# Optimization experiments

Hardware: AMD Instinct MI355X
Metric: run time of the kernel (lower is better)

Reference implementation:

```python
import jax, jax.numpy as jnp
import numpy as np

B, L, T = 256, 256, 50  # batch, max_len, num_tags


def setup_inputs() -> dict:
    key = jax.random.key(0)
    k1, k2, k3 = jax.random.split(key, 3)
    feats = jax.random.normal(k1, (B, L, T), dtype=jnp.float32)
    trans_m = jax.random.normal(k2, (T, T), dtype=jnp.float32)
    tags = jax.random.randint(k3, (B, L), 0, T)
    mask = jnp.ones((B, L), dtype=jnp.int32)
    return {"feats": feats, "trans_m": trans_m, "tags": tags, "mask": mask}


def _normalizer(logits, trans_m, m):
    # logits: (L, B, T), m: (L, B) float mask
    alpha0 = logits[0]  # (B, T)

    def step(alpha, inp):
        emit, mt = inp  # (B, T), (B,)
        # (B, T_from, T_to) broadcast add, logsumexp over T_from
        tmp = alpha[:, :, None] + trans_m[None, :, :] + emit[:, None, :]
        new = jax.nn.logsumexp(tmp, axis=1)
        alpha = jnp.where(mt[:, None] > 0, new, alpha)
        return alpha, None

    alpha, _ = jax.lax.scan(step, alpha0, (logits[1:], m[1:]))
    return jax.nn.logsumexp(alpha, axis=1)  # (B,)


def _gold_score(logits, trans_m, tags_t, m):
    # logits: (L, B, T); tags_t: (L, B); m: (L, B)
    trans_sc = trans_m[tags_t[:-1], tags_t[1:]] * m[1:]  # (L-1, B)
    emit_sc = jnp.take_along_axis(logits, tags_t[:, :, None], axis=2)[..., 0] * m  # (L, B)
    return jnp.sum(trans_sc + emit_sc[:-1], axis=0) + emit_sc[-1]  # (B,)


def reference(feats, trans_m, tags, mask):
    # feats: (B, L, T) -> (L, B, T); include_start_end_trans=False
    logits = jnp.transpose(feats, (1, 0, 2))
    tags_t = tags.T
    m = mask.T.astype(feats.dtype)
    all_path = _normalizer(logits, trans_m, m)
    gold = _gold_score(logits, trans_m, tags_t, m)
    return all_path - gold  # (B,) loss per example
```

## Files before the change

### kernel.cpp

```cpp
#include <hip/hip_runtime.h>
#include <math.h>


#define TAGS 50
#define LEN 256
#define NB 256
#define VST 32
#define NCH 6
#define CST 32
#define INV_LN2 1.4426950408889634f
#define LN2 0.6931471805599453f

typedef __attribute__((ext_vector_type(8))) short bf16x8;
typedef __attribute__((ext_vector_type(4))) float f32x4;

#if __has_builtin(__builtin_amdgcn_exp2f)
#define EXP2F(x) __builtin_amdgcn_exp2f(x)
#else
#define EXP2F(x) exp2f(x)
#endif
#if __has_builtin(__builtin_amdgcn_logf)
#define LOG2F(x) __builtin_amdgcn_logf(x)
#else
#define LOG2F(x) log2f(x)
#endif
#if __has_builtin(__builtin_amdgcn_rcpf)
#define RCPF(x) __builtin_amdgcn_rcpf(x)
#else
#define RCPF(x) (1.0f / (x))
#endif

__device__ __forceinline__ float readlane_f(float v, int srclane) {
  return __builtin_bit_cast(float,
      __builtin_amdgcn_readlane(__builtin_bit_cast(int, v), srclane));
}

__device__ __forceinline__ int bfpack(float lo, float hi) {
  unsigned lb = __builtin_bit_cast(unsigned, lo) + 0x8000u;
  unsigned hb = __builtin_bit_cast(unsigned, hi) + 0x8000u;
#if __has_builtin(__builtin_amdgcn_perm)
  return (int)__builtin_amdgcn_perm(hb, lb, 0x07060302u);
#else
  return (int)((hb & 0xFFFF0000u) | (lb >> 16));
#endif
}

union U8 { int i[4]; bf16x8 v; };

#define WS_U(b)    ((b) * 64)
#define WS_W(b)    ((NB + (b)) * 64)
#define WS_SF(b)   (2 * NB * 64 + (b))
#define WS_SB(b)   (2 * NB * 64 + NB + (b))
#define WS_SC(b,c) (2 * NB * 64 + 2 * NB + (b) * NCH + (c))
#define WS_T(b,c)  (2 * NB * 64 + 2 * NB + NB * NCH + (((b) * NCH + (c)) * 64) * 64)

__global__ __launch_bounds__(64, 1) void crf_scan_kernel(
    const float* __restrict__ feats,
    const float* __restrict__ trans,
    const int*   __restrict__ mask,
    float*       __restrict__ ws)
{
  const int bid  = blockIdx.x;
  const int lane = threadIdx.x;
  const int q    = lane >> 4;
  const int n    = lane & 15;
  const f32x4 zero4 = {0.0f, 0.0f, 0.0f, 0.0f};

  if (bid < 2 * NB) {
    const bool is_fwd = bid < NB;
    const int b = is_fwd ? bid : bid - NB;

    __shared__ __align__(16) float fl[VST * TAGS];
    __shared__ int ml[VST];

    const int base_l = is_fwd ? 0 : (LEN - VST);
    const float* fb = feats + ((size_t)b * LEN + base_l) * TAGS;
    const int*   mb = mask + b * LEN + base_l;

    {
      const float4* fv = (const float4*)fb;
      for (int i = lane; i < (VST * TAGS) / 4; i += 64) {
        float4 v4 = fv[i];
        v4.x *= INV_LN2; v4.y *= INV_LN2; v4.z *= INV_LN2; v4.w *= INV_LN2;
        *(float4*)&fl[i * 4] = v4;
      }
      for (int i = lane; i < VST; i += 64) ml[i] = mb[i];
    }

    int tcl[4], vld[4];
#pragma unroll
    for (int t = 0; t < 4; ++t) {
      const int tg = n + 16 * t;
      vld[t] = tg < TAGS;
      tcl[t] = vld[t] ? tg : (TAGS - 1);
    }

    U8 Bfr[4][2];
#pragma unroll
    for (int t = 0; t < 4; ++t)
#pragma unroll
      for (int c = 0; c < 2; ++c)
#pragma unroll
        for (int r = 0; r < 4; ++r) {
          const int col = 16 * t + n;
          const int tag0 = 16 * c + 4 * q + r;
          const int tag1 = tag0 + 32;
          float e0 = 0.0f, e1 = 0.0f;
          if (col < TAGS) {
            if (tag0 < TAGS)
              e0 = EXP2F((is_fwd ? trans[tag0 * TAGS + col]
                                 : trans[col * TAGS + tag0]) * INV_LN2);
            if (tag1 < TAGS)
              e1 = EXP2F((is_fwd ? trans[tag1 * TAGS + col]
                                 : trans[col * TAGS + tag1]) * INV_LN2);
          }
          Bfr[t][c].i[r] = bfpack(e0, e1);
        }

    int addr[4];
#pragma unroll
    for (int r = 0; r < 4; ++r) addr[r] = (4 * q + r) * 4;

    __syncthreads();

    float v[4], S;
    if (is_fwd) {
      const float c0 = fl[0];
#pragma unroll
      for (int t = 0; t < 4; ++t) v[t] = vld[t] ? EXP2F(fl[tcl[t]] - c0) : 0.0f;
      S = c0;
      float eh[4];
#pragma unroll
      for (int t = 0; t < 4; ++t) eh[t] = EXP2F(fl[TAGS + tcl[t]]);
      int m_nxt = ml[1];

      for (int l = 1; l < VST; ++l) {
        const int m_cur = m_nxt;
        const int ln = (l + 1 < VST) ? (l + 1) : (VST - 1);
        const int P0 = bfpack(v[0], v[2]);
        const int P1 = bfpack(v[1], v[3]);
        const float cc = readlane_f(v[0], 0);
        const float rr = RCPF(cc);
        U8 A0, A1;
#pragma unroll
        for (int r = 0; r < 4; ++r) {
          A0.i[r] = __builtin_amdgcn_ds_bpermute(addr[r], P0);
          A1.i[r] = __builtin_amdgcn_ds_bpermute(addr[r], P1);
        }
        f32x4 d0 = __builtin_amdgcn_mfma_f32_16x16x32_bf16(A0.v, Bfr[0][0].v, zero4, 0, 0, 0);
        f32x4 d1 = __builtin_amdgcn_mfma_f32_16x16x32_bf16(A0.v, Bfr[1][0].v, zero4, 0, 0, 0);
        f32x4 d2 = __builtin_amdgcn_mfma_f32_16x16x32_bf16(A0.v, Bfr[2][0].v, zero4, 0, 0, 0);
        f32x4 d3 = __builtin_amdgcn_mfma_f32_16x16x32_bf16(A0.v, Bfr[3][0].v, zero4, 0, 0, 0);
        f32x4 g0 = __builtin_amdgcn_mfma_f32_16x16x32_bf16(A1.v, Bfr[0][1].v, zero4, 0, 0, 0);
        f32x4 g1 = __builtin_amdgcn_mfma_f32_16x16x32_bf16(A1.v, Bfr[1][1].v, zero4, 0, 0, 0);
        f32x4 g2 = __builtin_amdgcn_mfma_f32_16x16x32_bf16(A1.v, Bfr[2][1].v, zero4, 0, 0, 0);
        f32x4 g3 = __builtin_amdgcn_mfma_f32_16x16x32_bf16(A1.v, Bfr[3][1].v, zero4, 0, 0, 0);
        float ehn[4];
#pragma unroll
        for (int t = 0; t < 4; ++t) ehn[t] = fl[ln * TAGS + tcl[t]];
        const int m_n2 = ml[ln];
        v[0] = ((m_cur > 0) ? (d0[0] + g0[0]) * eh[0] : v[0]) * rr;
        v[1] = ((m_cur > 0) ? (d1[0] + g1[0]) * eh[1] : v[1]) * rr;
        v[2] = ((m_cur > 0) ? (d2[0] + g2[0]) * eh[2] : v[2]) * rr;
        v[3] = ((m_cur > 0) ? (d3[0] + g3[0]) * eh[3] : v[3]) * rr;
        S += LOG2F(cc);
#pragma unroll
        for (int t = 0; t < 4; ++t) eh[t] = EXP2F(ehn[t]);
        m_nxt = m_n2;
      }
      if (lane < 16) {
#pragma unroll
        for (int t = 0; t < 4; ++t) ws[WS_U(b) + n + 16 * t] = v[t];
      }
      if (lane == 0) ws[WS_SF(b)] = S;
    } else {
#pragma unroll
      for (int t = 0; t < 4; ++t) v[t] = vld[t] ? 1.0f : 0.0f;
      S = 0.0f;
      float eh[4];
#pragma unroll
      for (int t = 0; t < 4; ++t) eh[t] = EXP2F(fl[(VST - 1) * TAGS + tcl[t]]);
      int m_nxt = ml[VST - 1];

      for (int l = VST - 1; l >= 0; --l) {
        const int m_cur = m_nxt;
        const int ln = (l > 0) ? (l - 1) : 0;
        const float x0 = v[0] * eh[0];
        const float x1 = v[1] * eh[1];
        const float x2 = v[2] * eh[2];
        const float x3 = v[3] * eh[3];
        const int P0 = bfpack(x0, x2);
        const int P1 = bfpack(x1, x3);
        const float cc = readlane_f(v[0], 0);
        const float rr = RCPF(cc);
        U8 A0, A1;
#pragma unroll
        for (int r = 0; r < 4; ++r) {
          A0.i[r] = __builtin_amdgcn_ds_bpermute(addr[r], P0);
          A1.i[r] = __builtin_amdgcn_ds_bpermute(addr[r], P1);
        }
        f32x4 d0 = __builtin_amdgcn_mfma_f32_16x16x32_bf16(A0.v, Bfr[0][0].v, zero4, 0, 0, 0);
        f32x4 d1 = __builtin_amdgcn_mfma_f32_16x16x32_bf16(A0.v, Bfr[1][0].v, zero4, 0, 0, 0);
        f32x4 d2 = __builtin_amdgcn_mfma_f32_16x16x32_bf16(A0.v, Bfr[2][0].v, zero4, 0, 0, 0);
        f32x4 d3 = __builtin_amdgcn_mfma_f32_16x16x32_bf16(A0.v, Bfr[3][0].v, zero4, 0, 0, 0);
        f32x4 g0 = __builtin_amdgcn_mfma_f32_16x16x32_bf16(A1.v, Bfr[0][1].v, zero4, 0, 0, 0);
        f32x4 g1 = __builtin_amdgcn_mfma_f32_16x16x32_bf16(A1.v, Bfr[1][1].v, zero4, 0, 0, 0);
        f32x4 g2 = __builtin_amdgcn_mfma_f32_16x16x32_bf16(A1.v, Bfr[2][1].v, zero4, 0, 0, 0);
        f32x4 g3 = __builtin_amdgcn_mfma_f32_16x16x32_bf16(A1.v, Bfr[3][1].v, zero4, 0, 0, 0);
        float ehn[4];
#pragma unroll
        for (int t = 0; t < 4; ++t) ehn[t] = fl[ln * TAGS + tcl[t]];
        const int m_n2 = ml[ln];
        v[0] = ((m_cur > 0) ? (d0[0] + g0[0]) : v[0]) * rr;
        v[1] = ((m_cur > 0) ? (d1[0] + g1[0]) : v[1]) * rr;
        v[2] = ((m_cur > 0) ? (d2[0] + g2[0]) : v[2]) * rr;
        v[3] = ((m_cur > 0) ? (d3[0] + g3[0]) : v[3]) * rr;
        S += LOG2F(cc);
#pragma unroll
        for (int t = 0; t < 4; ++t) eh[t] = EXP2F(ehn[t]);
        m_nxt = m_n2;
      }
      if (lane < 16) {
#pragma unroll
        for (int t = 0; t < 4; ++t) ws[WS_W(b) + n + 16 * t] = v[t];
      }
      if (lane == 0) ws[WS_SB(b)] = S;
    }
    return;
  }

  {
    const int i2 = bid - 2 * NB;
    const int b = i2 / NCH;
    const int cidx = i2 - b * NCH;
    const int l0 = CST * (cidx + 1);

    __shared__ __align__(16) float em[CST * 52 + 16];
    __shared__ int ml[CST];

    for (int i = lane; i < CST * 52 + 16; i += 64) em[i] = 0.0f;
    __syncthreads();

    const float* fbc = feats + ((size_t)b * LEN + l0) * TAGS;
    {
      const float4* fv = (const float4*)fbc;
      for (int i = lane; i < (CST * TAGS) / 4; i += 64) {
        const float4 v4 = fv[i];
        const int g = i * 4;
#pragma unroll
        for (int e = 0; e < 4; ++e) {
          const int gg = g + e;
          const int row = gg / TAGS;
          const int col = gg - row * TAGS;
          const float val = (e == 0) ? v4.x : (e == 1) ? v4.y : (e == 2) ? v4.z : v4.w;
          em[row * 52 + col] = val * INV_LN2;
        }
      }
      for (int i = lane; i < CST; i += 64) ml[i] = mask[b * LEN + l0 + i];
    }

    U8 Afr[4][2];
#pragma unroll
    for (int tm = 0; tm < 4; ++tm)
#pragma unroll
      for (int c2 = 0; c2 < 2; ++c2)
#pragma unroll
        for (int rr = 0; rr < 4; ++rr) {
          const int m = 16 * tm + n;
          const int kr = 32 * c2 + 16 * (rr >> 1) + 4 * q + 2 * (rr & 1);
          const float e0 = (m < TAGS && kr < TAGS)
              ? EXP2F(trans[kr * TAGS + m] * INV_LN2) : 0.0f;
          const float e1 = (m < TAGS && kr + 1 < TAGS)
              ? EXP2F(trans[(kr + 1) * TAGS + m] * INV_LN2) : 0.0f;
          Afr[tm][c2].i[rr] = bfpack(e0, e1);
        }

    __syncthreads();

    f32x4 d[4][4];
#pragma unroll
    for (int tm = 0; tm < 4; ++tm)
#pragma unroll
      for (int tn = 0; tn < 4; ++tn)
#pragma unroll
        for (int e = 0; e < 4; ++e)
          d[tm][tn][e] = (tm == tn && n == 4 * q + e) ? 1.0f : 0.0f;

    float S = 0.0f;

    for (int l = 0; l < CST; ++l) {
      if (ml[l] > 0) {
        const float cc = readlane_f(d[0][0][0], 0);
        const float rv = RCPF(cc);

        U8 Bf[2][4];
#pragma unroll
        for (int c2 = 0; c2 < 2; ++c2)
#pragma unroll
          for (int tn = 0; tn < 4; ++tn) {
            Bf[c2][tn].i[0] = bfpack(d[2 * c2][tn][0], d[2 * c2][tn][1]);
            Bf[c2][tn].i[1] = bfpack(d[2 * c2][tn][2], d[2 * c2][tn][3]);
            Bf[c2][tn].i[2] = bfpack(d[2 * c2 + 1][tn][0], d[2 * c2 + 1][tn][1]);
            Bf[c2][tn].i[3] = bfpack(d[2 * c2 + 1][tn][2], d[2 * c2 + 1][tn][3]);
          }

        float sc[4][4];
#pragma unroll
        for (int tm = 0; tm < 4; ++tm) {
          const f32x4 er = *(const f32x4*)&em[l * 52 + 16 * tm + 4 * q];
#pragma unroll
          for (int e = 0; e < 4; ++e) sc[tm][e] = EXP2F(er[e]) * rv;
        }

#pragma unroll
        for (int tm = 0; tm < 4; ++tm)
#pragma unroll
          for (int tn = 0; tn < 4; ++tn) {
            f32x4 acc = __builtin_amdgcn_mfma_f32_16x16x32_bf16(
                Afr[tm][0].v, Bf[0][tn].v, zero4, 0, 0, 0);
            acc = __builtin_amdgcn_mfma_f32_16x16x32_bf16(
                Afr[tm][1].v, Bf[1][tn].v, acc, 0, 0, 0);
#pragma unroll
            for (int e = 0; e < 4; ++e) d[tm][tn][e] = acc[e] * sc[tm][e];
          }
        S += LOG2F(cc);
      }
    }

    float* tw = ws + WS_T(b, cidx);
#pragma unroll
    for (int tm = 0; tm < 4; ++tm)
#pragma unroll
      for (int tn = 0; tn < 4; ++tn)
#pragma unroll
        for (int e = 0; e < 4; ++e)
          tw[(16 * tn + n) * 64 + 16 * tm + 4 * q + e] = d[tm][tn][e];
    if (lane == 0) ws[WS_SC(b, cidx)] = S;
  }
}

__global__ __launch_bounds__(64) void crf_combine_kernel(
    const float* __restrict__ feats,
    const float* __restrict__ trans,
    const int*   __restrict__ tags,
    const int*   __restrict__ mask,
    const float* __restrict__ ws,
    float*       __restrict__ out)
{
  const int b = blockIdx.x;
  const int lane = threadIdx.x;

  float x = ws[WS_U(b) + lane];
  float Ssum = 0.0f;

  for (int c = 0; c < NCH; ++c) {
    const float* Tb = ws + WS_T(b, c) + lane;
    float a0 = 0.0f, a1 = 0.0f, a2 = 0.0f, a3 = 0.0f;
#pragma unroll
    for (int i = 0; i < 64; i += 4) {
      a0 = fmaf(Tb[(i + 0) * 64], readlane_f(x, i + 0), a0);
      a1 = fmaf(Tb[(i + 1) * 64], readlane_f(x, i + 1), a1);
      a2 = fmaf(Tb[(i + 2) * 64], readlane_f(x, i + 2), a2);
      a3 = fmaf(Tb[(i + 3) * 64], readlane_f(x, i + 3), a3);
    }
    const float acc = (a0 + a1) + (a2 + a3);
    const float cc = readlane_f(acc, 0);
    x = acc * RCPF(cc);
    Ssum += LOG2F(cc) + ws[WS_SC(b, c)];
  }

  float s = x * ws[WS_W(b) + lane];
#pragma unroll
  for (int off = 32; off; off >>= 1) s += __shfl_xor(s, off, 64);

  const float* fb = feats + (size_t)b * (LEN * TAGS);
  const int*   tb = tags + b * LEN;
  const int*   mb = mask + b * LEN;
  float gp = 0.0f;
#pragma unroll
  for (int k = 0; k < 4; ++k) {
    const int p = lane + 64 * k;
    const int tg = tb[p];
    if (mb[p] > 0) {
      float vv = fb[p * TAGS + tg];
      if (p >= 1) vv += trans[tb[p - 1] * TAGS + tg];
      gp += vv;
    }
  }
#pragma unroll
  for (int off = 32; off; off >>= 1) gp += __shfl_xor(gp, off, 64);

  if (lane == 0) {
    const float Sf = ws[WS_SF(b)];
    const float Sb = ws[WS_SB(b)];
    out[b] = LN2 * (Sf + Sb + Ssum + LOG2F(s)) - gp;
  }
}

extern "C" void kernel_launch(void* const* d_in, const int* in_sizes, int n_in,
                              void* d_out, int out_size, void* d_ws, size_t ws_size,
                              hipStream_t stream) {
  const float* feats = (const float*)d_in[0];
  const float* trans = (const float*)d_in[1];
  const int*   tags  = (const int*)d_in[2];
  const int*   mask  = (const int*)d_in[3];
  float* out = (float*)d_out;
  float* ws  = (float*)d_ws;

  crf_scan_kernel<<<2 * NB + NB * NCH, 64, 0, stream>>>(feats, trans, mask, ws);
  crf_combine_kernel<<<NB, 64, 0, stream>>>(feats, trans, tags, mask, ws, out);
}
```

Measured before the change: 126.8 us.

## Split chunk transfer-matrix products across four blocks by column group

Result: slower. 139.4 us (+9.9%).

```diff
diff --git a/kernel.cpp b/kernel.cpp
--- a/kernel.cpp
+++ b/kernel.cpp
@@ -47,14 +47,14 @@
 
 union U8 { int i[4]; bf16x8 v; };
 
-#define WS_U(b)    ((b) * 64)
-#define WS_W(b)    ((NB + (b)) * 64)
-#define WS_SF(b)   (2 * NB * 64 + (b))
-#define WS_SB(b)   (2 * NB * 64 + NB + (b))
-#define WS_SC(b,c) (2 * NB * 64 + 2 * NB + (b) * NCH + (c))
-#define WS_T(b,c)  (2 * NB * 64 + 2 * NB + NB * NCH + (((b) * NCH + (c)) * 64) * 64)
-
-__global__ __launch_bounds__(64, 1) void crf_scan_kernel(
+#define WS_U(b)     ((b) * 64)
+#define WS_W(b)     ((NB + (b)) * 64)
+#define WS_SF(b)    (2 * NB * 64 + (b))
+#define WS_SB(b)    (2 * NB * 64 + NB + (b))
+#define WS_SC4(b,c) (2 * NB * 64 + 2 * NB + ((b) * NCH + (c)) * 4)
+#define WS_T(b,c)   (2 * NB * 64 + 2 * NB + NB * NCH * 4 + (((b) * NCH + (c)) * 64) * 64)
+
+__global__ __launch_bounds__(64) void crf_scan_kernel(
     const float* __restrict__ feats,
     const float* __restrict__ trans,
     const int*   __restrict__ mask,
@@ -231,14 +231,16 @@
 
   {
     const int i2 = bid - 2 * NB;
-    const int b = i2 / NCH;
-    const int cidx = i2 - b * NCH;
+    const int b = i2 / (NCH * 4);
+    const int rem = i2 - b * (NCH * 4);
+    const int cidx = rem >> 2;
+    const int w = rem & 3;
     const int l0 = CST * (cidx + 1);
 
-    __shared__ __align__(16) float em[CST * 52 + 16];
+    __shared__ __align__(16) float eh[CST * 52 + 16];
     __shared__ int ml[CST];
 
-    for (int i = lane; i < CST * 52 + 16; i += 64) em[i] = 0.0f;
+    for (int i = lane; i < CST * 52 + 16; i += 64) eh[i] = 1.0f;
     __syncthreads();
 
     const float* fbc = feats + ((size_t)b * LEN + l0) * TAGS;
@@ -253,7 +255,7 @@
           const int row = gg / TAGS;
           const int col = gg - row * TAGS;
           const float val = (e == 0) ? v4.x : (e == 1) ? v4.y : (e == 2) ? v4.z : v4.w;
-          em[row * 52 + col] = val * INV_LN2;
+          eh[row * 52 + col] = EXP2F(val * INV_LN2);
         }
       }
       for (int i = lane; i < CST; i += 64) ml[i] = mask[b * LEN + l0 + i];
@@ -277,65 +279,53 @@
 
     __syncthreads();
 
-    f32x4 d[4][4];
+    f32x4 d[4];
 #pragma unroll
     for (int tm = 0; tm < 4; ++tm)
 #pragma unroll
-      for (int tn = 0; tn < 4; ++tn)
-#pragma unroll
-        for (int e = 0; e < 4; ++e)
-          d[tm][tn][e] = (tm == tn && n == 4 * q + e) ? 1.0f : 0.0f;
+      for (int e = 0; e < 4; ++e)
+        d[tm][e] = (tm == w && (4 * q + e) == n) ? 1.0f : 0.0f;
 
     float S = 0.0f;
 
     for (int l = 0; l < CST; ++l) {
       if (ml[l] > 0) {
-        const float cc = readlane_f(d[0][0][0], 0);
+        float pvt = d[0][0];
+        pvt = (w == 1) ? d[1][0] : pvt;
+        pvt = (w == 2) ? d[2][0] : pvt;
+        pvt = (w == 3) ? d[3][0] : pvt;
+        const float cc = readlane_f(pvt, 0);
         const float rv = RCPF(cc);
 
-        U8 Bf[2][4];
-#pragma unroll
-        for (int c2 = 0; c2 < 2; ++c2)
-#pragma unroll
-          for (int tn = 0; tn < 4; ++tn) {
-            Bf[c2][tn].i[0] = bfpack(d[2 * c2][tn][0], d[2 * c2][tn][1]);
-            Bf[c2][tn].i[1] = bfpack(d[2 * c2][tn][2], d[2 * c2][tn][3]);
-            Bf[c2][tn].i[2] = bfpack(d[2 * c2 + 1][tn][0], d[2 * c2 + 1][tn][1]);
-            Bf[c2][tn].i[3] = bfpack(d[2 * c2 + 1][tn][2], d[2 * c2 + 1][tn][3]);
-          }
-
-        float sc[4][4];
+        U8 B0, B1;
+        B0.i[0] = bfpack(d[0][0], d[0][1]);
+        B0.i[1] = bfpack(d[0][2], d[0][3]);
+        B0.i[2] = bfpack(d[1][0], d[1][1]);
+        B0.i[3] = bfpack(d[1][2], d[1][3]);
+        B1.i[0] = bfpack(d[2][0], d[2][1]);
+        B1.i[1] = bfpack(d[2][2], d[2][3]);
+        B1.i[2] = bfpack(d[3][0], d[3][1]);
+        B1.i[3] = bfpack(d[3][2], d[3][3]);
+
 #pragma unroll
         for (int tm = 0; tm < 4; ++tm) {
-          const f32x4 er = *(const f32x4*)&em[l * 52 + 16 * tm + 4 * q];
-#pragma unroll
-          for (int e = 0; e < 4; ++e) sc[tm][e] = EXP2F(er[e]) * rv;
-        }
-
-#pragma unroll
-        for (int tm = 0; tm < 4; ++tm)
-#pragma unroll
-          for (int tn = 0; tn < 4; ++tn) {
-            f32x4 acc = __builtin_amdgcn_mfma_f32_16x16x32_bf16(
-                Afr[tm][0].v, Bf[0][tn].v, zero4, 0, 0, 0);
-            acc = __builtin_amdgcn_mfma_f32_16x16x32_bf16(
-                Afr[tm][1].v, Bf[1][tn].v, acc, 0, 0, 0);
-#pragma unroll
-            for (int e = 0; e < 4; ++e) d[tm][tn][e] = acc[e] * sc[tm][e];
-          }
+          f32x4 acc = __builtin_amdgcn_mfma_f32_16x16x32_bf16(
+              Afr[tm][0].v, B0.v, zero4, 0, 0, 0);
+          acc = __builtin_amdgcn_mfma_f32_16x16x32_bf16(
+              Afr[tm][1].v, B1.v, acc, 0, 0, 0);
+          const f32x4 er = *(const f32x4*)&eh[l * 52 + 16 * tm + 4 * q];
+#pragma unroll
+          for (int e = 0; e < 4; ++e) d[tm][e] = acc[e] * (er[e] * rv);
+        }
         S += LOG2F(cc);
       }
     }
 
-    float* tw = ws + WS_T(b, cidx);
+    float* tw = ws + WS_T(b, cidx) + (16 * w + n) * 64;
 #pragma unroll
     for (int tm = 0; tm < 4; ++tm)
-#pragma unroll
-      for (int tn = 0; tn < 4; ++tn)
-#pragma unroll
-        for (int e = 0; e < 4; ++e)
-          tw[(16 * tn + n) * 64 + 16 * tm + 4 * q + e] = d[tm][tn][e];
-    if (lane == 0) ws[WS_SC(b, cidx)] = S;
+      *(f32x4*)&tw[16 * tm + 4 * q] = d[tm];
+    if (lane == 0) ws[WS_SC4(b, cidx) + w] = S;
   }
 }
 
@@ -354,6 +344,11 @@
   float Ssum = 0.0f;
 
   for (int c = 0; c < NCH; ++c) {
+    const float sw = ws[WS_SC4(b, c) + (lane >> 4)];
+    float m1 = fmaxf(sw, __shfl_xor(sw, 16, 64));
+    const float smax = fmaxf(m1, __shfl_xor(m1, 32, 64));
+    x *= EXP2F(sw - smax);
+
     const float* Tb = ws + WS_T(b, c) + lane;
     float a0 = 0.0f, a1 = 0.0f, a2 = 0.0f, a3 = 0.0f;
 #pragma unroll
@@ -366,7 +361,7 @@
     const float acc = (a0 + a1) + (a2 + a3);
     const float cc = readlane_f(acc, 0);
     x = acc * RCPF(cc);
-    Ssum += LOG2F(cc) + ws[WS_SC(b, c)];
+    Ssum += smax + LOG2F(cc);
   }
 
   float s = x * ws[WS_W(b) + lane];
@@ -407,6 +402,6 @@
   float* out = (float*)d_out;
   float* ws  = (float*)d_ws;
 
-  crf_scan_kernel<<<2 * NB + NB * NCH, 64, 0, stream>>>(feats, trans, mask, ws);
+  crf_scan_kernel<<<2 * NB + NB * NCH * 4, 64, 0, stream>>>(feats, trans, mask, ws);
   crf_combine_kernel<<<NB, 64, 0, stream>>>(feats, trans, tags, mask, ws, out);
 }
```
